# Kernel optimization log

Measured on AMD Instinct MI355X. Metric: run time of the kernel, lower is better.

Reference implementation:

```python
import jax, jax.numpy as jnp
import numpy as np

N = 65536          # number of active voxels
GRID = 96          # sparse volume side
P = 4              # cardinality (paths)
KS = 3             # kernel size per dim
K = KS ** 3        # 27 kernel offsets
DILS = [1, 3, 9, 27]
C_IN = 128
C_PATH = 32        # in/out features per path = 128 / 4
BN_EPS = 1e-5
LEAK = 0.0


def _build_kernel_maps():
    """Build padded gather/scatter maps per (path, kernel offset).

    in_map[p,k,:] / out_map[p,k,:]: out[out_idx] += W[k] @ x[in_idx].
    Padded with sentinel index N (maps to a zero row / dumped row).
    """
    rng = np.random.default_rng(0)
    flat = rng.choice(GRID ** 3, size=N, replace=False)
    coords = np.stack(np.unravel_index(flat, (GRID, GRID, GRID)), axis=1)  # [N,3]
    order = np.argsort(flat)
    sorted_keys = flat[order]
    offs = np.array([[dx, dy, dz] for dx in (-1, 0, 1)
                     for dy in (-1, 0, 1) for dz in (-1, 0, 1)])
    in_map = np.full((P, K, N), N, dtype=np.int32)
    out_map = np.full((P, K, N), N, dtype=np.int32)
    for p in range(P):
        d = DILS[p]
        for k in range(K):
            nb = coords + offs[k] * d
            valid = np.all((nb >= 0) & (nb < GRID), axis=1)
            nbkey = nb[:, 0] * GRID * GRID + nb[:, 1] * GRID + nb[:, 2]
            pos = np.clip(np.searchsorted(sorted_keys, nbkey), 0, N - 1)
            hit = valid & (sorted_keys[pos] == nbkey)
            j = np.nonzero(hit)[0]
            in_map[p, k, :j.size] = order[pos[j]].astype(np.int32)
            out_map[p, k, :j.size] = j.astype(np.int32)
    return jnp.asarray(in_map), jnp.asarray(out_map)


def setup_inputs() -> dict:
    key = jax.random.key(0)
    ks = jax.random.split(key, 4)
    in_map, out_map = _build_kernel_maps()
    return {
        "feats": jax.random.normal(ks[0], (N, C_IN), jnp.float32),
        "lin_W": jax.random.normal(ks[1], (P, C_IN, C_PATH), jnp.float32) * 0.05,
        "lin_b": jnp.zeros((P, C_PATH), jnp.float32),
        "conv_W": jax.random.normal(ks[2], (P, K, C_PATH, C_PATH), jnp.float32) * 0.05,
        "gamma": jnp.ones((P, C_PATH), jnp.float32),
        "beta": jnp.zeros((P, C_PATH), jnp.float32),
        "fin_W": jax.random.normal(ks[3], (C_IN, C_IN), jnp.float32) * 0.05,
        "fin_b": jnp.zeros((C_IN,), jnp.float32),
        "in_map": in_map,
        "out_map": out_map,
    }


def _sparse_conv(x, W, im, om):
    """x: [N,C]; W: [K,C,Co]; im/om: [K,N] padded index maps."""
    n = x.shape[0]
    co = W.shape[2]
    xp = jnp.concatenate([x, jnp.zeros((1, x.shape[1]), x.dtype)], axis=0)
    gathered = xp[im]                                   # [K,N,C]
    contrib = jnp.einsum('knc,kcd->knd', gathered, W)   # [K,N,Co]
    out = jnp.zeros((n + 1, co), x.dtype)
    out = out.at[om.reshape(-1)].add(contrib.reshape(-1, co))
    return out[:n]


def reference(feats, lin_W, lin_b, conv_W, gamma, beta, fin_W, fin_b,
              in_map, out_map):
    outs = []
    for p in range(P):
        h = feats @ lin_W[p] + lin_b[p]                 # MinkowskiLinear
        h = _sparse_conv(h, conv_W[p], in_map[p], out_map[p])
        mu = h.mean(axis=0)                             # BN (training stats)
        var = h.var(axis=0)
        h = (h - mu) * jax.lax.rsqrt(var + BN_EPS) * gamma[p] + beta[p]
        h = jax.nn.leaky_relu(h, LEAK)
        outs.append(h)
    cat = jnp.concatenate(outs, axis=1)                 # [N, 128]
    out = cat @ fin_W + fin_b + feats                   # linear + residual (identity)
    return out
```

## Files before the change

### kernel.cpp

```cpp
#include <hip/hip_runtime.h>


#define NN    65536
#define CIN   128
#define CPATH 32
#define NPATH 4
#define NK    27
#define TJ    512
#define NTILE (NN / TJ)

typedef __attribute__((ext_vector_type(8))) short bfx8;
typedef __attribute__((ext_vector_type(4))) float fx4;

__device__ __forceinline__ unsigned short f2bf(float f) {
    unsigned u = __builtin_bit_cast(unsigned, f);
    u += 0x7FFFu + ((u >> 16) & 1u);
    return (unsigned short)(u >> 16);
}
__device__ __forceinline__ float bf2f(unsigned short s) {
    return __builtin_bit_cast(float, (unsigned)s << 16);
}
__device__ __forceinline__ bfx8 pack_bf8(const float4 a, const float4 b) {
    union { unsigned short s[8]; bfx8 v; } u;
    u.s[0] = f2bf(a.x); u.s[1] = f2bf(a.y); u.s[2] = f2bf(a.z); u.s[3] = f2bf(a.w);
    u.s[4] = f2bf(b.x); u.s[5] = f2bf(b.y); u.s[6] = f2bf(b.z); u.s[7] = f2bf(b.w);
    return u.v;
}

__global__ void wprep_rng(const float* __restrict__ convW,
                          const float* __restrict__ linW,
                          const float* __restrict__ finW,
                          const int* __restrict__ om,
                          unsigned short* __restrict__ Wt,
                          unsigned short* __restrict__ Wlt,
                          unsigned short* __restrict__ Wft,
                          unsigned short* __restrict__ Hb,
                          int* __restrict__ rngAll) {
    const int b = blockIdx.x;
    const int t = threadIdx.x;
    if (b < 108) {
        if (b == 0 && t < 64)
            ((unsigned*)(Hb + (size_t)NN * CIN))[t] = 0u;
        const int m = t >> 3;
        const int c0 = (t & 7) * 4;
        const float4 w = *(const float4*)(convW + ((size_t)b * CPATH + m) * CPATH + c0);
        unsigned short* o = Wt + (size_t)b * CPATH * CPATH;
        o[(c0 + 0) * CPATH + m] = f2bf(w.x);
        o[(c0 + 1) * CPATH + m] = f2bf(w.y);
        o[(c0 + 2) * CPATH + m] = f2bf(w.z);
        o[(c0 + 3) * CPATH + m] = f2bf(w.w);
    } else if (b < 112) {
        const int col = (b - 108) * 32 + (t >> 3);
        const int p = col >> 5, c = col & 31;
        const int k0 = (t & 7) * 16;
        for (int k = k0; k < k0 + 16; k++)
            Wlt[col * CIN + k] = f2bf(linW[(size_t)p * CIN * CPATH + k * CPATH + c]);
    } else if (b < 116) {
        const int col = (b - 112) * 32 + (t >> 3);
        const int k0 = (t & 7) * 16;
        for (int k = k0; k < k0 + 16; k++)
            Wft[col * CIN + k] = f2bf(finW[(size_t)k * CIN + col]);
    } else {
        const int idx = (b - 116) * 256 + t;
        if (idx < NPATH * NK * (NTILE + 1)) {
            const int tile = idx % (NTILE + 1);
            const int pk = idx / (NTILE + 1);
            const int bound = tile * TJ;
            const int* o = om + (size_t)pk * NN;
            int lo = 0, hi = NN;
            while (lo < hi) {
                const int mid = (lo + hi) >> 1;
                if (o[mid] < bound) lo = mid + 1; else hi = mid;
            }
            rngAll[idx] = lo;
        }
    }
}

__global__ void __launch_bounds__(256, 4)
lin_mfma(const float* __restrict__ feats,
         const unsigned short* __restrict__ Wlt,
         const float* __restrict__ linb,
         unsigned short* __restrict__ Hb) {
    const int tid = threadIdx.x;
    const int w = tid >> 6, lane = tid & 63;
    const int mrow = lane & 15, kq = lane >> 4;
    const int row = blockIdx.x * 64 + w * 16 + mrow;

    fx4 acc[8];
#pragma unroll
    for (int g = 0; g < 8; g++) acc[g] = (fx4){0.f, 0.f, 0.f, 0.f};

#pragma unroll
    for (int kt = 0; kt < 4; ++kt) {
        const float4 y0 = *(const float4*)(feats + (size_t)row * CIN + kt * 32 + kq * 8);
        const float4 y1 = *(const float4*)(feats + (size_t)row * CIN + kt * 32 + kq * 8 + 4);
        const bfx8 yf = pack_bf8(y0, y1);
#pragma unroll
        for (int g = 0; g < 8; g++) {
            const bfx8 xf = *(const bfx8*)(Wlt + (size_t)(g * 16 + mrow) * CIN + kt * 32 + kq * 8);
            acc[g] = __builtin_amdgcn_mfma_f32_16x16x32_bf16(xf, yf, acc[g], 0, 0, 0);
        }
    }
#pragma unroll
    for (int g = 0; g < 8; g++) {
        const int c0 = g * 16 + kq * 4;
        const float4 bb = *(const float4*)(linb + c0);
        union { unsigned short s[4]; ushort4 v; } u;
        u.s[0] = f2bf(acc[g][0] + bb.x);
        u.s[1] = f2bf(acc[g][1] + bb.y);
        u.s[2] = f2bf(acc[g][2] + bb.z);
        u.s[3] = f2bf(acc[g][3] + bb.w);
        *(ushort4*)(Hb + (size_t)row * CIN + c0) = u.v;
    }
}

__global__ void __launch_bounds__(512, 4)
sconv7(const unsigned short* __restrict__ Hb,
       const unsigned short* __restrict__ Wt,
       const int* __restrict__ im,
       const int* __restrict__ om,
       const int* __restrict__ rngAll,
       unsigned short* __restrict__ Cbh,
       float* __restrict__ part) {
    __shared__ int idxT[TJ][29];
    __shared__ int rng[NK][2];
    __shared__ float red[8][64];

    const int p = blockIdx.y;
    const int T = blockIdx.x;
    const int j0 = T * TJ;
    const int tid = threadIdx.x;
    const int w = tid >> 6, lane = tid & 63;
    const int mrow = lane & 15, kq = lane >> 4;

    for (int idx = tid; idx < TJ * 29; idx += 512)
        (&idxT[0][0])[idx] = NN;
    if (tid < NK * 2) {
        const int k = tid >> 1, which = tid & 1;
        rng[k][which] = rngAll[((size_t)p * NK + k) * (NTILE + 1) + T + which];
    }
    __syncthreads();
    {
        const int k = tid >> 4;
        if (k < NK) {
            const int s = rng[k][0], e = rng[k][1];
            const int* ok = om + ((size_t)p * NK + k) * NN;
            const int* ik = im + ((size_t)p * NK + k) * NN;
            for (int t = s + (tid & 15); t < e; t += 16)
                idxT[ok[t] - j0][k] = ik[t];
        }
    }
    __syncthreads();

    fx4 acc[4][2];
#pragma unroll
    for (int f = 0; f < 4; f++)
#pragma unroll
        for (int h = 0; h < 2; h++) acc[f][h] = (fx4){0.f, 0.f, 0.f, 0.f};

    const unsigned short* Wp = Wt + (size_t)p * NK * 1024 + kq * 8;
    const unsigned short* Hp = Hb + (size_t)p * CPATH + kq * 8;
    const int rb = w * 64 + mrow;

#pragma unroll 3
    for (int k = 0; k < NK; ++k) {
        const bfx8 x0 = *(const bfx8*)(Wp + (size_t)k * 1024 + mrow * CPATH);
        const bfx8 x1 = *(const bfx8*)(Wp + (size_t)k * 1024 + (16 + mrow) * CPATH);
        const int i0 = idxT[rb +  0][k];
        const int i1 = idxT[rb + 16][k];
        const int i2 = idxT[rb + 32][k];
        const int i3 = idxT[rb + 48][k];
        const bfx8 y0 = *(const bfx8*)(Hp + (size_t)i0 * CIN);
        const bfx8 y1 = *(const bfx8*)(Hp + (size_t)i1 * CIN);
        const bfx8 y2 = *(const bfx8*)(Hp + (size_t)i2 * CIN);
        const bfx8 y3 = *(const bfx8*)(Hp + (size_t)i3 * CIN);
        acc[0][0] = __builtin_amdgcn_mfma_f32_16x16x32_bf16(x0, y0, acc[0][0], 0, 0, 0);
        acc[0][1] = __builtin_amdgcn_mfma_f32_16x16x32_bf16(x1, y0, acc[0][1], 0, 0, 0);
        acc[1][0] = __builtin_amdgcn_mfma_f32_16x16x32_bf16(x0, y1, acc[1][0], 0, 0, 0);
        acc[1][1] = __builtin_amdgcn_mfma_f32_16x16x32_bf16(x1, y1, acc[1][1], 0, 0, 0);
        acc[2][0] = __builtin_amdgcn_mfma_f32_16x16x32_bf16(x0, y2, acc[2][0], 0, 0, 0);
        acc[2][1] = __builtin_amdgcn_mfma_f32_16x16x32_bf16(x1, y2, acc[2][1], 0, 0, 0);
        acc[3][0] = __builtin_amdgcn_mfma_f32_16x16x32_bf16(x0, y3, acc[3][0], 0, 0, 0);
        acc[3][1] = __builtin_amdgcn_mfma_f32_16x16x32_bf16(x1, y3, acc[3][1], 0, 0, 0);
    }

    {
        float s[8], q[8];
#pragma unroll
        for (int h = 0; h < 2; h++)
#pragma unroll
            for (int r = 0; r < 4; r++) {
                float sv = 0.f, qv = 0.f;
#pragma unroll
                for (int f = 0; f < 4; f++) {
                    const float v = acc[f][h][r];
                    sv += v;
                    qv = fmaf(v, v, qv);
                }
                s[h * 4 + r] = sv;
                q[h * 4 + r] = qv;
            }
#pragma unroll
        for (int m = 1; m < 16; m <<= 1)
#pragma unroll
            for (int i = 0; i < 8; i++) {
                s[i] += __shfl_xor(s[i], m, 64);
                q[i] += __shfl_xor(q[i], m, 64);
            }
        if (mrow == 0) {
#pragma unroll
            for (int h = 0; h < 2; h++)
#pragma unroll
                for (int r = 0; r < 4; r++) {
                    const int c = h * 16 + kq * 4 + r;
                    red[w][c] = s[h * 4 + r];
                    red[w][32 + c] = q[h * 4 + r];
                }
        }
    }
    __syncthreads();
    if (tid < 64) {
        float sum = 0.f;
#pragma unroll
        for (int i = 0; i < 8; i++) sum += red[i][tid];
        part[(((size_t)p * NTILE) + T) * 64 + tid] = sum;
    }

#pragma unroll
    for (int f = 0; f < 4; f++) {
        const int row = j0 + w * 64 + f * 16 + mrow;
#pragma unroll
        for (int h = 0; h < 2; h++) {
            union { unsigned short s[4]; ushort4 v; } u;
            u.s[0] = f2bf(acc[f][h][0]);
            u.s[1] = f2bf(acc[f][h][1]);
            u.s[2] = f2bf(acc[f][h][2]);
            u.s[3] = f2bf(acc[f][h][3]);
            *(ushort4*)(Cbh + (size_t)row * CIN + p * CPATH + h * 16 + kq * 4) = u.v;
        }
    }
}

__global__ void bn_stats2(const float* __restrict__ part,
                          const float* __restrict__ gamma,
                          const float* __restrict__ beta,
                          float* __restrict__ ss) {
    __shared__ float rs[4][128], rq[4][128];
    const int c = threadIdx.x & 127;
    const int ch = threadIdx.x >> 7;
    const int p = c >> 5, cc = c & 31;
    float s = 0.f, s2 = 0.f;
    for (int t = ch * (NTILE / 4); t < (ch + 1) * (NTILE / 4); t++) {
        s += part[(((size_t)p * NTILE) + t) * 64 + cc];
        s2 += part[(((size_t)p * NTILE) + t) * 64 + 32 + cc];
    }
    rs[ch][c] = s;
    rq[ch][c] = s2;
    __syncthreads();
    if (ch == 0) {
        s = rs[0][c] + rs[1][c] + rs[2][c] + rs[3][c];
        s2 = rq[0][c] + rq[1][c] + rq[2][c] + rq[3][c];
        const float mean = s * (1.f / NN);
        const float var = s2 * (1.f / NN) - mean * mean;
        const float sc = gamma[c] * rsqrtf(var + 1e-5f);
        ss[c] = sc;
        ss[128 + c] = beta[c] - mean * sc;
    }
}

__global__ void __launch_bounds__(256, 4)
fin_mfma(const unsigned short* __restrict__ Cbh,
         const float* __restrict__ ss,
         const unsigned short* __restrict__ Wft,
         const float* __restrict__ finb,
         const float* __restrict__ feats,
         float* __restrict__ out) {
    const int tid = threadIdx.x;
    const int w = tid >> 6, lane = tid & 63;
    const int mrow = lane & 15, kq = lane >> 4;
    const int row = blockIdx.x * 64 + w * 16 + mrow;

    fx4 acc[8];
#pragma unroll
    for (int g = 0; g < 8; g++) acc[g] = (fx4){0.f, 0.f, 0.f, 0.f};

#pragma unroll
    for (int kt = 0; kt < 4; ++kt) {
        const int k0 = kt * 32 + kq * 8;
        union { unsigned short s[8]; bfx8 v; } cb;
        cb.v = *(const bfx8*)(Cbh + (size_t)row * CIN + k0);
        const float4 sc0 = *(const float4*)(ss + k0);
        const float4 sc1 = *(const float4*)(ss + k0 + 4);
        const float4 sh0 = *(const float4*)(ss + 128 + k0);
        const float4 sh1 = *(const float4*)(ss + 128 + k0 + 4);
        float4 a, b;
        a.x = fmaxf(fmaf(bf2f(cb.s[0]), sc0.x, sh0.x), 0.f);
        a.y = fmaxf(fmaf(bf2f(cb.s[1]), sc0.y, sh0.y), 0.f);
        a.z = fmaxf(fmaf(bf2f(cb.s[2]), sc0.z, sh0.z), 0.f);
        a.w = fmaxf(fmaf(bf2f(cb.s[3]), sc0.w, sh0.w), 0.f);
        b.x = fmaxf(fmaf(bf2f(cb.s[4]), sc1.x, sh1.x), 0.f);
        b.y = fmaxf(fmaf(bf2f(cb.s[5]), sc1.y, sh1.y), 0.f);
        b.z = fmaxf(fmaf(bf2f(cb.s[6]), sc1.z, sh1.z), 0.f);
        b.w = fmaxf(fmaf(bf2f(cb.s[7]), sc1.w, sh1.w), 0.f);
        const bfx8 yf = pack_bf8(a, b);
#pragma unroll
        for (int g = 0; g < 8; g++) {
            const bfx8 xf = *(const bfx8*)(Wft + (size_t)(g * 16 + mrow) * CIN + kt * 32 + kq * 8);
            acc[g] = __builtin_amdgcn_mfma_f32_16x16x32_bf16(xf, yf, acc[g], 0, 0, 0);
        }
    }
#pragma unroll
    for (int g = 0; g < 8; g++) {
        const int c0 = g * 16 + kq * 4;
        const float4 fb = *(const float4*)(finb + c0);
        const float4 rs = *(const float4*)(feats + (size_t)row * CIN + c0);
        float4 o;
        o.x = acc[g][0] + fb.x + rs.x;
        o.y = acc[g][1] + fb.y + rs.y;
        o.z = acc[g][2] + fb.z + rs.z;
        o.w = acc[g][3] + fb.w + rs.w;
        *(float4*)(out + (size_t)row * CIN + c0) = o;
    }
}

extern "C" void kernel_launch(void* const* d_in, const int* in_sizes, int n_in,
                              void* d_out, int out_size, void* d_ws,
                              size_t ws_size, hipStream_t stream) {
    (void)in_sizes; (void)n_in; (void)out_size; (void)ws_size;
    const float* feats = (const float*)d_in[0];
    const float* linW  = (const float*)d_in[1];
    const float* linb  = (const float*)d_in[2];
    const float* convW = (const float*)d_in[3];
    const float* gamma = (const float*)d_in[4];
    const float* beta  = (const float*)d_in[5];
    const float* finW  = (const float*)d_in[6];
    const float* finb  = (const float*)d_in[7];
    const int*   im    = (const int*)d_in[8];
    const int*   om    = (const int*)d_in[9];
    float* out = (float*)d_out;

    char* ws = (char*)d_ws;
    unsigned short* Hb  = (unsigned short*)(ws);
    unsigned short* Cbh = (unsigned short*)(ws + 16781312);
    unsigned short* Wt  = (unsigned short*)(ws + 33558528);
    unsigned short* Wlt = (unsigned short*)(ws + 33779712);
    unsigned short* Wft = (unsigned short*)(ws + 33812480);
    int*   rngAll       = (int*)(ws + 33845248);
    float* part         = (float*)(ws + 33902592);
    float* ss           = (float*)(ws + 34033664);

    const int rng_total = NPATH * NK * (NTILE + 1);
    const int rng_blocks = (rng_total + 255) / 256;
    wprep_rng<<<116 + rng_blocks, 256, 0, stream>>>(convW, linW, finW, om,
                                                    Wt, Wlt, Wft, Hb, rngAll);
    lin_mfma<<<1024, 256, 0, stream>>>(feats, Wlt, linb, Hb);
    sconv7<<<dim3(NTILE, NPATH), 512, 0, stream>>>(Hb, Wt, im, om, rngAll, Cbh, part);
    bn_stats2<<<1, 512, 0, stream>>>(part, gamma, beta, ss);
    fin_mfma<<<1024, 256, 0, stream>>>(Cbh, ss, Wft, finb, feats, out);
}
```

Before: 108.3 us.

## Shrink sparse-conv tiles to 128 rows and split output channels across waves

Cuts the sparse-conv row tile from 512 to 128 and uses 256-thread blocks. Each wave now owns 64 rows and one 16-channel half of the outputs, so it issues four MFMAs per kernel offset instead of eight. This gives 4x more blocks and lower register pressure (launch bounds 256,6), which should improve occupancy and latency hiding for the gathered loads. In exchange, each gathered row is fetched by two waves and there are more partial BN sums for the stats kernel to reduce. The workspace offsets for the partial-stats buffer are moved to fit the larger rngAll array.

```diff
diff --git a/kernel.cpp b/kernel.cpp
--- a/kernel.cpp
+++ b/kernel.cpp
@@ -6,7 +6,7 @@
 #define CPATH 32
 #define NPATH 4
 #define NK    27
-#define TJ    512
+#define TJ    128
 #define NTILE (NN / TJ)
 
 typedef __attribute__((ext_vector_type(8))) short bfx8;
@@ -115,8 +115,8 @@
     }
 }
 
-__global__ void __launch_bounds__(512, 4)
-sconv7(const unsigned short* __restrict__ Hb,
+__global__ void __launch_bounds__(256, 6)
+sconv9(const unsigned short* __restrict__ Hb,
        const unsigned short* __restrict__ Wt,
        const int* __restrict__ im,
        const int* __restrict__ om,
@@ -125,7 +125,7 @@
        float* __restrict__ part) {
     __shared__ int idxT[TJ][29];
     __shared__ int rng[NK][2];
-    __shared__ float red[8][64];
+    __shared__ float red[4][64];
 
     const int p = blockIdx.y;
     const int T = blockIdx.x;
@@ -133,8 +133,10 @@
     const int tid = threadIdx.x;
     const int w = tid >> 6, lane = tid & 63;
     const int mrow = lane & 15, kq = lane >> 4;
-
-    for (int idx = tid; idx < TJ * 29; idx += 512)
+    const int g = w & 1, hs = w >> 1;
+
+    ((float*)red)[tid] = 0.f;
+    for (int idx = tid; idx < TJ * 29; idx += 256)
         (&idxT[0][0])[idx] = NN;
     if (tid < NK * 2) {
         const int k = tid >> 1, which = tid & 1;
@@ -142,31 +144,28 @@
     }
     __syncthreads();
     {
-        const int k = tid >> 4;
+        const int k = tid >> 3;
         if (k < NK) {
             const int s = rng[k][0], e = rng[k][1];
             const int* ok = om + ((size_t)p * NK + k) * NN;
             const int* ik = im + ((size_t)p * NK + k) * NN;
-            for (int t = s + (tid & 15); t < e; t += 16)
+            for (int t = s + (tid & 7); t < e; t += 8)
                 idxT[ok[t] - j0][k] = ik[t];
         }
     }
     __syncthreads();
 
-    fx4 acc[4][2];
-#pragma unroll
-    for (int f = 0; f < 4; f++)
-#pragma unroll
-        for (int h = 0; h < 2; h++) acc[f][h] = (fx4){0.f, 0.f, 0.f, 0.f};
-
-    const unsigned short* Wp = Wt + (size_t)p * NK * 1024 + kq * 8;
+    fx4 acc[4];
+#pragma unroll
+    for (int f = 0; f < 4; f++) acc[f] = (fx4){0.f, 0.f, 0.f, 0.f};
+
+    const unsigned short* Wp = Wt + (size_t)p * NK * 1024 + (hs * 16 + mrow) * CPATH + kq * 8;
     const unsigned short* Hp = Hb + (size_t)p * CPATH + kq * 8;
-    const int rb = w * 64 + mrow;
+    const int rb = g * 64 + mrow;
 
 #pragma unroll 3
     for (int k = 0; k < NK; ++k) {
-        const bfx8 x0 = *(const bfx8*)(Wp + (size_t)k * 1024 + mrow * CPATH);
-        const bfx8 x1 = *(const bfx8*)(Wp + (size_t)k * 1024 + (16 + mrow) * CPATH);
+        const bfx8 x = *(const bfx8*)(Wp + (size_t)k * 1024);
         const int i0 = idxT[rb +  0][k];
         const int i1 = idxT[rb + 16][k];
         const int i2 = idxT[rb + 32][k];
@@ -175,70 +174,57 @@
         const bfx8 y1 = *(const bfx8*)(Hp + (size_t)i1 * CIN);
         const bfx8 y2 = *(const bfx8*)(Hp + (size_t)i2 * CIN);
         const bfx8 y3 = *(const bfx8*)(Hp + (size_t)i3 * CIN);
-        acc[0][0] = __builtin_amdgcn_mfma_f32_16x16x32_bf16(x0, y0, acc[0][0], 0, 0, 0);
-        acc[0][1] = __builtin_amdgcn_mfma_f32_16x16x32_bf16(x1, y0, acc[0][1], 0, 0, 0);
-        acc[1][0] = __builtin_amdgcn_mfma_f32_16x16x32_bf16(x0, y1, acc[1][0], 0, 0, 0);
-        acc[1][1] = __builtin_amdgcn_mfma_f32_16x16x32_bf16(x1, y1, acc[1][1], 0, 0, 0);
-        acc[2][0] = __builtin_amdgcn_mfma_f32_16x16x32_bf16(x0, y2, acc[2][0], 0, 0, 0);
-        acc[2][1] = __builtin_amdgcn_mfma_f32_16x16x32_bf16(x1, y2, acc[2][1], 0, 0, 0);
-        acc[3][0] = __builtin_amdgcn_mfma_f32_16x16x32_bf16(x0, y3, acc[3][0], 0, 0, 0);
-        acc[3][1] = __builtin_amdgcn_mfma_f32_16x16x32_bf16(x1, y3, acc[3][1], 0, 0, 0);
+        acc[0] = __builtin_amdgcn_mfma_f32_16x16x32_bf16(x, y0, acc[0], 0, 0, 0);
+        acc[1] = __builtin_amdgcn_mfma_f32_16x16x32_bf16(x, y1, acc[1], 0, 0, 0);
+        acc[2] = __builtin_amdgcn_mfma_f32_16x16x32_bf16(x, y2, acc[2], 0, 0, 0);
+        acc[3] = __builtin_amdgcn_mfma_f32_16x16x32_bf16(x, y3, acc[3], 0, 0, 0);
     }
 
     {
-        float s[8], q[8];
-#pragma unroll
-        for (int h = 0; h < 2; h++)
+        float s[4], q[4];
+#pragma unroll
+        for (int r = 0; r < 4; r++) {
+            float sv = 0.f, qv = 0.f;
+#pragma unroll
+            for (int f = 0; f < 4; f++) {
+                const float v = acc[f][r];
+                sv += v;
+                qv = fmaf(v, v, qv);
+            }
+            s[r] = sv;
+            q[r] = qv;
+        }
+#pragma unroll
+        for (int m = 1; m < 16; m <<= 1)
 #pragma unroll
             for (int r = 0; r < 4; r++) {
-                float sv = 0.f, qv = 0.f;
-#pragma unroll
-                for (int f = 0; f < 4; f++) {
-                    const float v = acc[f][h][r];
-                    sv += v;
-                    qv = fmaf(v, v, qv);
-                }
-                s[h * 4 + r] = sv;
-                q[h * 4 + r] = qv;
-            }
-#pragma unroll
-        for (int m = 1; m < 16; m <<= 1)
-#pragma unroll
-            for (int i = 0; i < 8; i++) {
-                s[i] += __shfl_xor(s[i], m, 64);
-                q[i] += __shfl_xor(q[i], m, 64);
+                s[r] += __shfl_xor(s[r], m, 64);
+                q[r] += __shfl_xor(q[r], m, 64);
             }
         if (mrow == 0) {
 #pragma unroll
-            for (int h = 0; h < 2; h++)
-#pragma unroll
-                for (int r = 0; r < 4; r++) {
-                    const int c = h * 16 + kq * 4 + r;
-                    red[w][c] = s[h * 4 + r];
-                    red[w][32 + c] = q[h * 4 + r];
-                }
+            for (int r = 0; r < 4; r++) {
+                const int c = hs * 16 + kq * 4 + r;
+                red[w][c] = s[r];
+                red[w][32 + c] = q[r];
+            }
         }
     }
     __syncthreads();
     if (tid < 64) {
-        float sum = 0.f;
-#pragma unroll
-        for (int i = 0; i < 8; i++) sum += red[i][tid];
-        part[(((size_t)p * NTILE) + T) * 64 + tid] = sum;
+        part[(((size_t)p * NTILE) + T) * 64 + tid] =
+            red[0][tid] + red[1][tid] + red[2][tid] + red[3][tid];
     }
 
 #pragma unroll
     for (int f = 0; f < 4; f++) {
-        const int row = j0 + w * 64 + f * 16 + mrow;
-#pragma unroll
-        for (int h = 0; h < 2; h++) {
-            union { unsigned short s[4]; ushort4 v; } u;
-            u.s[0] = f2bf(acc[f][h][0]);
-            u.s[1] = f2bf(acc[f][h][1]);
-            u.s[2] = f2bf(acc[f][h][2]);
-            u.s[3] = f2bf(acc[f][h][3]);
-            *(ushort4*)(Cbh + (size_t)row * CIN + p * CPATH + h * 16 + kq * 4) = u.v;
-        }
+        const int row = j0 + g * 64 + f * 16 + mrow;
+        union { unsigned short s[4]; ushort4 v; } u;
+        u.s[0] = f2bf(acc[f][0]);
+        u.s[1] = f2bf(acc[f][1]);
+        u.s[2] = f2bf(acc[f][2]);
+        u.s[3] = f2bf(acc[f][3]);
+        *(ushort4*)(Cbh + (size_t)row * CIN + p * CPATH + hs * 16 + kq * 4) = u.v;
     }
 }
 
@@ -347,15 +333,15 @@
     unsigned short* Wlt = (unsigned short*)(ws + 33779712);
     unsigned short* Wft = (unsigned short*)(ws + 33812480);
     int*   rngAll       = (int*)(ws + 33845248);
-    float* part         = (float*)(ws + 33902592);
-    float* ss           = (float*)(ws + 34033664);
+    float* part         = (float*)(ws + 34074624);
+    float* ss           = (float*)(ws + 34598912);
 
     const int rng_total = NPATH * NK * (NTILE + 1);
     const int rng_blocks = (rng_total + 255) / 256;
     wprep_rng<<<116 + rng_blocks, 256, 0, stream>>>(convW, linW, finW, om,
                                                     Wt, Wlt, Wft, Hb, rngAll);
     lin_mfma<<<1024, 256, 0, stream>>>(feats, Wlt, linb, Hb);
-    sconv7<<<dim3(NTILE, NPATH), 512, 0, stream>>>(Hb, Wt, im, om, rngAll, Cbh, part);
+    sconv9<<<dim3(NTILE, NPATH), 256, 0, stream>>>(Hb, Wt, im, om, rngAll, Cbh, part);
     bn_stats2<<<1, 512, 0, stream>>>(part, gamma, beta, ss);
     fin_mfma<<<1024, 256, 0, stream>>>(Cbh, ss, Wft, finb, feats, out);
 }
```

New measurement: 152.3 us. 1.41x slower.
